# Performance work log

Hardware: AMD Instinct MI355X
Metric: run time of the kernel (lower is better)

The kernel has to match this reference:

```python
import jax, jax.numpy as jnp
import numpy as np

N = 25000          # nodes
E = 400000         # edges (avg degree 16)
H = 64             # hidden_nf
TYPE_DIM = 1
NL = 5             # 4 gcl layers + dgcl_0 (identical shapes, stacked)
GROUP = jnp.array([[[1., 0.], [0., 1.]], [[-1., 0.], [0., -1.]]], dtype=jnp.float32)  # [G,2,2]


def setup_inputs() -> dict:
    key = jax.random.key(0)
    ks = iter(jax.random.split(key, 40))
    def nrm(shape, scale=0.05):
        return jax.random.normal(next(ks), shape, dtype=jnp.float32) * scale
    inp = {}
    inp["nodes"] = nrm((N, 4 + TYPE_DIM), 1.0)
    inp["edges"] = jax.random.randint(next(ks), (2, E), 0, N)
    inp["edge_attr"] = nrm((E, 1), 1.0)
    # embedding: Linear(input_dim, H)
    inp["W_emb"] = nrm((4 + TYPE_DIM, H)); inp["b_emb"] = jnp.zeros((H,), jnp.float32)
    # group_mlp: Linear(G*H, H) -> SiLU -> Linear(H, H)
    G = GROUP.shape[0]
    inp["Wg1"] = nrm((G * H, H)); inp["bg1"] = jnp.zeros((H,), jnp.float32)
    inp["Wg2"] = nrm((H, H));     inp["bg2"] = jnp.zeros((H,), jnp.float32)
    # stacked GCL params for gcl_0..3 + dgcl_0 (all H->H, edges_in_nf=1)
    inp["eW1"] = nrm((NL, 2 * H + 1, H)); inp["eb1"] = jnp.zeros((NL, H), jnp.float32)
    inp["eW2"] = nrm((NL, H, H));         inp["eb2"] = jnp.zeros((NL, H), jnp.float32)
    inp["nW1"] = nrm((NL, 2 * H, H));     inp["nb1"] = jnp.zeros((NL, H), jnp.float32)
    inp["nW2"] = nrm((NL, H, H));         inp["nb2"] = jnp.zeros((NL, H), jnp.float32)
    # dgcl_1: GCL(H, 2*len(group)=4, H)
    inp["deW1"] = nrm((2 * H + 1, H)); inp["deb1"] = jnp.zeros((H,), jnp.float32)
    inp["deW2"] = nrm((H, H));         inp["deb2"] = jnp.zeros((H,), jnp.float32)
    inp["dnW1"] = nrm((2 * H, H));     inp["dnb1"] = jnp.zeros((H,), jnp.float32)
    inp["dnW2"] = nrm((H, 2 * G));     inp["dnb2"] = jnp.zeros((2 * G,), jnp.float32)
    return inp


def _gcl(h, row, col, edge_attr, eW1, eb1, eW2, eb2, nW1, nb1, nW2, nb2):
    # edge model: gather -> MLP (Linear,SiLU,Linear,SiLU)
    e_in = jnp.concatenate([h[row], h[col], edge_attr], axis=1)  # [E, 2H+1]
    e = jax.nn.silu(e_in @ eW1 + eb1)
    e = jax.nn.silu(e @ eW2 + eb2)                               # [E, H]
    # node model: scatter-sum by source index, then MLP (Linear,SiLU,Linear)
    agg = jax.ops.segment_sum(e, row, num_segments=h.shape[0])   # [N, H]
    out = jnp.concatenate([h, agg], axis=1)                      # [N, 2H]
    out = jax.nn.silu(out @ nW1 + nb1) @ nW2 + nb2
    return out  # recurrent=False: no residual


def reference(nodes, edges, edge_attr, W_emb, b_emb, Wg1, bg1, Wg2, bg2,
              eW1, eb1, eW2, eb2, nW1, nb1, nW2, nb2,
              deW1, deb1, deW2, deb2, dnW1, dnb1, dnW2, dnb2):
    loc, vel, ntype = nodes[:, :2], nodes[:, 2:4], nodes[:, 4:]
    # group-equivariant embedding: transform loc/vel by each group element
    loc_g = jnp.einsum('nd,gde->gne', loc, GROUP)   # [G, N, 2]
    vel_g = jnp.einsum('nd,gde->gne', vel, GROUP)   # [G, N, 2]
    ntype_g = jnp.broadcast_to(ntype, (GROUP.shape[0],) + ntype.shape)
    feats = jnp.concatenate([loc_g, vel_g, ntype_g], axis=2)   # [G, N, 5]
    h_g = feats @ W_emb + b_emb                                 # [G, N, H]
    h = jnp.transpose(h_g, (1, 0, 2)).reshape(nodes.shape[0], -1)  # [N, G*H]
    h = jax.nn.silu(h @ Wg1 + bg1) @ Wg2 + bg2
    row, col = edges[0], edges[1]
    for i in range(eW1.shape[0]):  # gcl_0..3 then dgcl_0
        h = _gcl(h, row, col, edge_attr, eW1[i], eb1[i], eW2[i], eb2[i],
                 nW1[i], nb1[i], nW2[i], nb2[i])
    # dgcl_1: node output dim = 2*len(group)
    x = _gcl(h, row, col, edge_attr, deW1, deb1, deW2, deb2,
             dnW1, dnb1, dnW2, dnb2)
    return x
```

## Files before the change

### kernel.cpp

```cpp
#include <hip/hip_runtime.h>
#include <hip/hip_bf16.h>

#define N_NODES 25000
#define N_EDGES 400000
#define NB_SCAN ((N_NODES + 255) / 256)
#define EDGE_TILES (N_EDGES / 16)
#define TPW 3
#define EDGE_WAVES ((EDGE_TILES + TPW - 1) / TPW)
#define EDGE_BLOCKS ((EDGE_WAVES + 3) / 4)
#define NODE_TILES ((N_NODES + 15) / 16)

typedef __attribute__((ext_vector_type(8))) short short8;
typedef __attribute__((ext_vector_type(4))) float f32x4;

__device__ __forceinline__ float silu_f(float x) {
  return x * __builtin_amdgcn_rcpf(1.0f + __expf(-x));
}

__device__ __forceinline__ short f2bf_s(float x) {
  __hip_bfloat16 h = __float2bfloat16(x);
  return *reinterpret_cast<short*>(&h);
}
__device__ __forceinline__ float bf_s2f(short s) {
  __hip_bfloat16 h = *reinterpret_cast<__hip_bfloat16*>(&s);
  return __bfloat162float(h);
}

__device__ __forceinline__ void load_afrag(const float* T, int s, int quad, int n16,
                                           short8& ahi, short8& alo) {
#pragma unroll
  for (int j = 0; j < 8; ++j) {
    float tv = T[(s * 32 + quad * 8 + j) * 17 + n16];
    short hi = f2bf_s(tv);
    ahi[j] = hi;
    alo[j] = f2bf_s(tv - bf_s2f(hi));
  }
}
__device__ __forceinline__ void load_bfrag(const float* __restrict__ W, int k0, int col,
                                           short8& bhi, short8& blo) {
#pragma unroll
  for (int j = 0; j < 8; ++j) {
    float w = W[(k0 + j) * 64 + col];
    short hi = f2bf_s(w);
    bhi[j] = hi;
    blo[j] = f2bf_s(w - bf_s2f(hi));
  }
}
__device__ __forceinline__ f32x4 mfma3(short8 ahi, short8 alo, short8 bhi, short8 blo,
                                       f32x4 acc) {
  acc = __builtin_amdgcn_mfma_f32_16x16x32_bf16(ahi, bhi, acc, 0, 0, 0);
  acc = __builtin_amdgcn_mfma_f32_16x16x32_bf16(ahi, blo, acc, 0, 0, 0);
  acc = __builtin_amdgcn_mfma_f32_16x16x32_bf16(alo, bhi, acc, 0, 0, 0);
  return acc;
}

__global__ __launch_bounds__(256) void k_hist(const int* __restrict__ rows,
                                              int* __restrict__ counts)
{
  int stride = gridDim.x * blockDim.x;
  for (int e = blockIdx.x * blockDim.x + threadIdx.x; e < N_EDGES; e += stride)
    atomicAdd(&counts[rows[e]], 1);
}

__global__ __launch_bounds__(256) void k_scanA(const int* __restrict__ counts,
                                               int* __restrict__ bsum)
{
  __shared__ int sd[256];
  int t = threadIdx.x;
  int i = blockIdx.x * 256 + t;
  int x = (i < N_NODES) ? counts[i] : 0;
  sd[t] = x; __syncthreads();
  for (int d = 128; d > 0; d >>= 1) { if (t < d) sd[t] += sd[t + d]; __syncthreads(); }
  if (t == 0) bsum[blockIdx.x] = sd[0];
}

__global__ __launch_bounds__(128) void k_scanB(const int* __restrict__ bsum,
                                               int* __restrict__ boffs)
{
  __shared__ int buf[128];
  int t = threadIdx.x;
  int x = (t < NB_SCAN) ? bsum[t] : 0;
  buf[t] = x; __syncthreads();
  for (int d = 1; d < 128; d <<= 1) {
    int y = (t >= d) ? buf[t - d] : 0;
    __syncthreads();
    buf[t] += y;
    __syncthreads();
  }
  if (t < NB_SCAN) boffs[t] = buf[t] - x;
}

__global__ __launch_bounds__(256) void k_scanC(const int* __restrict__ counts,
                                               const int* __restrict__ boffs,
                                               int* __restrict__ cursor)
{
  __shared__ int buf[256];
  int t = threadIdx.x;
  int i = blockIdx.x * 256 + t;
  int x = (i < N_NODES) ? counts[i] : 0;
  buf[t] = x; __syncthreads();
  for (int d = 1; d < 256; d <<= 1) {
    int y = (t >= d) ? buf[t - d] : 0;
    __syncthreads();
    buf[t] += y;
    __syncthreads();
  }
  if (i < N_NODES) cursor[i] = boffs[blockIdx.x] + buf[t] - x;
}

__global__ __launch_bounds__(256) void k_scatter(
    const int* __restrict__ rows, const int* __restrict__ cols,
    const float* __restrict__ eatt, int* __restrict__ cursor,
    int* __restrict__ srow, int* __restrict__ scol, float* __restrict__ sea)
{
  int stride = gridDim.x * blockDim.x;
  for (int e = blockIdx.x * blockDim.x + threadIdx.x; e < N_EDGES; e += stride) {
    int r = rows[e];
    int pos = atomicAdd(&cursor[r], 1);
    srow[pos] = r;
    scol[pos] = cols[e];
    sea[pos] = eatt[e];
  }
}

__global__ __launch_bounds__(256, 2) void k_embed_fused(
    const float* __restrict__ nodes,
    const float* __restrict__ W_emb, const float* __restrict__ b_emb,
    const float* __restrict__ Wg1, const float* __restrict__ bg1,
    const float* __restrict__ Wg2, const float* __restrict__ bg2,
    const float* __restrict__ eW1_0, const float* __restrict__ eb1_0,
    float* __restrict__ h, float* __restrict__ u, float* __restrict__ v,
    float* __restrict__ agg)
{
  const int lane = threadIdx.x & 63;
  const int wv = threadIdx.x >> 6;
  const int n16 = lane & 15;
  const int quad = lane >> 4;
  const int col = wv * 16 + n16;

  short8 W1hi[4], W1lo[4], W2hi[2], W2lo[2], Uhi[2], Ulo[2], Vhi[2], Vlo[2];
#pragma unroll
  for (int s = 0; s < 4; ++s)
    load_bfrag(Wg1, s * 32 + quad * 8, col, W1hi[s], W1lo[s]);
#pragma unroll
  for (int s = 0; s < 2; ++s) {
    load_bfrag(Wg2, s * 32 + quad * 8, col, W2hi[s], W2lo[s]);
    load_bfrag(eW1_0, s * 32 + quad * 8, col, Uhi[s], Ulo[s]);
    load_bfrag(eW1_0 + 64 * 64, s * 32 + quad * 8, col, Vhi[s], Vlo[s]);
  }
  float bg1v = bg1[col], bg2v = bg2[col], ebv = eb1_0[col];
  float w0 = W_emb[0 * 64 + lane], w1 = W_emb[1 * 64 + lane],
        w2 = W_emb[2 * 64 + lane], w3 = W_emb[3 * 64 + lane],
        w4 = W_emb[4 * 64 + lane];
  float bev = b_emb[lane];

  __shared__ float Ta[128 * 17];
  __shared__ float Tt[64 * 17];
  __shared__ float Th[64 * 17];
  __shared__ float Tu[64 * 17];
  __shared__ float Tv[64 * 17];

  int n0 = blockIdx.x * 16;
#pragma unroll
  for (int e4 = 0; e4 < 4; ++e4) {
    int e = wv * 4 + e4;
    int n = min(n0 + e, N_NODES - 1);
    float x0 = nodes[n * 5 + 0], x1 = nodes[n * 5 + 1],
          x2 = nodes[n * 5 + 2], x3 = nodes[n * 5 + 3],
          x4 = nodes[n * 5 + 4];
    float base = bev + x4 * w4;
    float sv = x0 * w0 + x1 * w1 + x2 * w2 + x3 * w3;
    Ta[lane * 17 + e] = base + sv;
    Ta[(64 + lane) * 17 + e] = base - sv;
  }
  __syncthreads();

  f32x4 a1 = {};
#pragma unroll
  for (int s = 0; s < 4; ++s) {
    short8 ahi, alo;
    load_afrag(Ta, s, quad, n16, ahi, alo);
    a1 = mfma3(ahi, alo, W1hi[s], W1lo[s], a1);
  }
#pragma unroll
  for (int r = 0; r < 4; ++r)
    Tt[col * 17 + quad * 4 + r] = silu_f(a1[r] + bg1v);
  __syncthreads();

  f32x4 a2 = {};
#pragma unroll
  for (int s = 0; s < 2; ++s) {
    short8 ahi, alo;
    load_afrag(Tt, s, quad, n16, ahi, alo);
    a2 = mfma3(ahi, alo, W2hi[s], W2lo[s], a2);
  }
#pragma unroll
  for (int r = 0; r < 4; ++r)
    Th[col * 17 + quad * 4 + r] = a2[r] + bg2v;
  __syncthreads();

  f32x4 aU = {}, aV = {};
#pragma unroll
  for (int s = 0; s < 2; ++s) {
    short8 ahi, alo;
    load_afrag(Th, s, quad, n16, ahi, alo);
    aU = mfma3(ahi, alo, Uhi[s], Ulo[s], aU);
    aV = mfma3(ahi, alo, Vhi[s], Vlo[s], aV);
  }
#pragma unroll
  for (int r = 0; r < 4; ++r) {
    Tu[col * 17 + quad * 4 + r] = aU[r] + ebv;
    Tv[col * 17 + quad * 4 + r] = aV[r];
  }
  __syncthreads();

#pragma unroll
  for (int e4 = 0; e4 < 4; ++e4) {
    int e = wv * 4 + e4;
    int n = n0 + e;
    if (n < N_NODES) {
      h[n * 64 + lane] = Th[lane * 17 + e];
      u[n * 64 + lane] = Tu[lane * 17 + e];
      v[n * 64 + lane] = Tv[lane * 17 + e];
      agg[n * 64 + lane] = 0.f;
    }
  }
}

__global__ __launch_bounds__(256, 2) void k_postfused(
    float* __restrict__ h, float* __restrict__ agg,
    const float* __restrict__ nW1, const float* __restrict__ nb1,
    const float* __restrict__ nW2, const float* __restrict__ nb2,
    const float* __restrict__ eW1n, const float* __restrict__ eb1n,
    float* __restrict__ u, float* __restrict__ v)
{
  const int lane = threadIdx.x & 63;
  const int wv = threadIdx.x >> 6;
  const int n16 = lane & 15;
  const int quad = lane >> 4;
  const int col = wv * 16 + n16;

  short8 W1hi[4], W1lo[4], W2hi[2], W2lo[2], Uhi[2], Ulo[2], Vhi[2], Vlo[2];
#pragma unroll
  for (int s = 0; s < 4; ++s)
    load_bfrag(nW1, s * 32 + quad * 8, col, W1hi[s], W1lo[s]);
#pragma unroll
  for (int s = 0; s < 2; ++s) {
    load_bfrag(nW2, s * 32 + quad * 8, col, W2hi[s], W2lo[s]);
    load_bfrag(eW1n, s * 32 + quad * 8, col, Uhi[s], Ulo[s]);
    load_bfrag(eW1n + 64 * 64, s * 32 + quad * 8, col, Vhi[s], Vlo[s]);
  }
  float b1 = nb1[col], b2 = nb2[col], ebv = eb1n[col];

  __shared__ float Ta[128 * 17];
  __shared__ float Tt[64 * 17];
  __shared__ float Th[64 * 17];
  __shared__ float Tu[64 * 17];
  __shared__ float Tv[64 * 17];

  int n0 = blockIdx.x * 16;
#pragma unroll
  for (int e4 = 0; e4 < 4; ++e4) {
    int e = wv * 4 + e4;
    int n = min(n0 + e, N_NODES - 1);
    Ta[lane * 17 + e] = h[n * 64 + lane];
    Ta[(64 + lane) * 17 + e] = agg[n * 64 + lane];
  }
  __syncthreads();

  f32x4 a1 = {};
#pragma unroll
  for (int s = 0; s < 4; ++s) {
    short8 ahi, alo;
    load_afrag(Ta, s, quad, n16, ahi, alo);
    a1 = mfma3(ahi, alo, W1hi[s], W1lo[s], a1);
  }
#pragma unroll
  for (int r = 0; r < 4; ++r)
    Tt[col * 17 + quad * 4 + r] = silu_f(a1[r] + b1);
  __syncthreads();

  f32x4 a2 = {};
#pragma unroll
  for (int s = 0; s < 2; ++s) {
    short8 ahi, alo;
    load_afrag(Tt, s, quad, n16, ahi, alo);
    a2 = mfma3(ahi, alo, W2hi[s], W2lo[s], a2);
  }
#pragma unroll
  for (int r = 0; r < 4; ++r)
    Th[col * 17 + quad * 4 + r] = a2[r] + b2;
  __syncthreads();

  f32x4 aU = {}, aV = {};
#pragma unroll
  for (int s = 0; s < 2; ++s) {
    short8 ahi, alo;
    load_afrag(Th, s, quad, n16, ahi, alo);
    aU = mfma3(ahi, alo, Uhi[s], Ulo[s], aU);
    aV = mfma3(ahi, alo, Vhi[s], Vlo[s], aV);
  }
#pragma unroll
  for (int r = 0; r < 4; ++r) {
    Tu[col * 17 + quad * 4 + r] = aU[r] + ebv;
    Tv[col * 17 + quad * 4 + r] = aV[r];
  }
  __syncthreads();

#pragma unroll
  for (int e4 = 0; e4 < 4; ++e4) {
    int e = wv * 4 + e4;
    int n = n0 + e;
    if (n < N_NODES) {
      h[n * 64 + lane] = Th[lane * 17 + e];
      u[n * 64 + lane] = Tu[lane * 17 + e];
      v[n * 64 + lane] = Tv[lane * 17 + e];
      agg[n * 64 + lane] = 0.f;
    }
  }
}

__global__ __launch_bounds__(256) void k_edge(
    const float* __restrict__ u, const float* __restrict__ v,
    const int* __restrict__ srow, const int* __restrict__ scol,
    const float* __restrict__ sea,
    const float* __restrict__ wea,
    const float* __restrict__ W2, const float* __restrict__ eb2,
    float* __restrict__ agg)
{
  const int lane = threadIdx.x & 63;
  const int wv = threadIdx.x >> 6;
  const int n16 = lane & 15;
  const int quad = lane >> 4;

  short8 Whi[2][4], Wlo[2][4];
#pragma unroll
  for (int s = 0; s < 2; ++s) {
#pragma unroll
    for (int nt = 0; nt < 4; ++nt) {
#pragma unroll
      for (int j = 0; j < 8; ++j) {
        float w2v = W2[(s * 32 + quad * 8 + j) * 64 + nt * 16 + n16];
        short hi = f2bf_s(w2v);
        Whi[s][nt][j] = hi;
        Wlo[s][nt][j] = f2bf_s(w2v - bf_s2f(hi));
      }
    }
  }
  float we = wea[lane];
  float b2v[4];
#pragma unroll
  for (int nt = 0; nt < 4; ++nt) b2v[nt] = eb2[nt * 16 + n16];

  __shared__ float Tl[4][64 * 17];
  float* T = Tl[wv];

  const int wid = blockIdx.x * 4 + wv;
  const int tile0 = wid * TPW;
  const int tile1 = min(tile0 + TPW, EDGE_TILES);

  int cur_row = -1;
  bool first_atomic = true;
  float asum[4] = {0.f, 0.f, 0.f, 0.f};

  int r_prev = -1;
  float uval = 0.f;

  auto reduce_pick = [&](float a0, float a1, float a2, float a3) -> float {
    a0 += __shfl_xor(a0, 16); a0 += __shfl_xor(a0, 32);
    a1 += __shfl_xor(a1, 16); a1 += __shfl_xor(a1, 32);
    a2 += __shfl_xor(a2, 16); a2 += __shfl_xor(a2, 32);
    a3 += __shfl_xor(a3, 16); a3 += __shfl_xor(a3, 32);
    float o = a0;
    o = (quad == 1) ? a1 : o;
    o = (quad == 2) ? a2 : o;
    o = (quad == 3) ? a3 : o;
    return o;
  };

  for (int tile = tile0; tile < tile1; ++tile) {
    int e0 = tile * 16;
    int r16a = srow[e0 + n16];
    int c16a = scol[e0 + n16];
    float ea16 = sea[e0 + n16];

    float vv[16];
#pragma unroll
    for (int e = 0; e < 16; ++e) {
      int c = __builtin_amdgcn_readlane(c16a, e);
      vv[e] = v[c * 64 + lane];
    }

#pragma unroll
    for (int e = 0; e < 16; ++e) {
      int r = __builtin_amdgcn_readlane(r16a, e);
      if (r != r_prev) { uval = u[r * 64 + lane]; r_prev = r; }
      float ea = __int_as_float(__builtin_amdgcn_readlane(__float_as_int(ea16), e));
      float tt = uval + vv[e] + ea * we;
      T[lane * 17 + e] = silu_f(tt);
    }
    __builtin_amdgcn_wave_barrier();

    f32x4 acc[4] = {};
#pragma unroll
    for (int s = 0; s < 2; ++s) {
      short8 ahi, alo;
#pragma unroll
      for (int j = 0; j < 8; ++j) {
        float tv = T[(s * 32 + quad * 8 + j) * 17 + n16];
        short hi = f2bf_s(tv);
        ahi[j] = hi;
        alo[j] = f2bf_s(tv - bf_s2f(hi));
      }
#pragma unroll
      for (int nt = 0; nt < 4; ++nt) {
        acc[nt] = __builtin_amdgcn_mfma_f32_16x16x32_bf16(ahi, Whi[s][nt], acc[nt], 0, 0, 0);
        acc[nt] = __builtin_amdgcn_mfma_f32_16x16x32_bf16(ahi, Wlo[s][nt], acc[nt], 0, 0, 0);
        acc[nt] = __builtin_amdgcn_mfma_f32_16x16x32_bf16(alo, Whi[s][nt], acc[nt], 0, 0, 0);
      }
    }
    __builtin_amdgcn_wave_barrier();

    float ev[4][4];
#pragma unroll
    for (int reg = 0; reg < 4; ++reg)
#pragma unroll
      for (int nt = 0; nt < 4; ++nt)
        ev[reg][nt] = silu_f(acc[nt][reg] + b2v[nt]);

    int rup = __shfl_up(r16a, 1);
    bool nf = (lane < 16) && ((lane == 0) ? (r16a != cur_row) : (r16a != rup));
    unsigned mask = (unsigned)(__ballot(nf) & 0xFFFFull);

    int s = 0;
    while (s < 16) {
      if ((mask >> s) & 1u) {
        if (cur_row >= 0) {
          float o = reduce_pick(asum[0], asum[1], asum[2], asum[3]);
          if (first_atomic) { unsafeAtomicAdd(&agg[cur_row * 64 + lane], o); first_atomic = false; }
          else agg[cur_row * 64 + lane] = o;
        }
        asum[0] = asum[1] = asum[2] = asum[3] = 0.f;
        cur_row = __shfl(r16a, s);
      }
      unsigned rem = mask & ~((2u << s) - 1u);
      int e = rem ? (__ffs(rem) - 1) : 16;
#pragma unroll
      for (int reg = 0; reg < 4; ++reg) {
        int m = quad * 4 + reg;
        bool in = (m >= s) && (m < e);
        asum[0] += in ? ev[reg][0] : 0.f;
        asum[1] += in ? ev[reg][1] : 0.f;
        asum[2] += in ? ev[reg][2] : 0.f;
        asum[3] += in ? ev[reg][3] : 0.f;
      }
      s = e;
    }
    __builtin_amdgcn_wave_barrier();
  }

  if (cur_row >= 0) {
    float o = reduce_pick(asum[0], asum[1], asum[2], asum[3]);
    unsafeAtomicAdd(&agg[cur_row * 64 + lane], o);
  }
}

__global__ __launch_bounds__(256, 2) void k_final_mfma(
    const float* __restrict__ h, const float* __restrict__ agg,
    const float* __restrict__ dnW1, const float* __restrict__ dnb1,
    const float* __restrict__ dnW2, const float* __restrict__ dnb2,
    float* __restrict__ out)
{
  const int lane = threadIdx.x & 63;
  const int wv = threadIdx.x >> 6;
  const int n16 = lane & 15;
  const int quad = lane >> 4;
  const int col = wv * 16 + n16;

  short8 W1hi[4], W1lo[4];
#pragma unroll
  for (int s = 0; s < 4; ++s)
    load_bfrag(dnW1, s * 32 + quad * 8, col, W1hi[s], W1lo[s]);
  float b1 = dnb1[col];

  __shared__ float Ta[128 * 17];
  __shared__ float Tt[64 * 17];
  __shared__ float W2s[256];
  __shared__ float Tp[4][64];

  W2s[threadIdx.x] = dnW2[threadIdx.x];

  int n0 = blockIdx.x * 16;
#pragma unroll
  for (int e4 = 0; e4 < 4; ++e4) {
    int e = wv * 4 + e4;
    int n = min(n0 + e, N_NODES - 1);
    Ta[lane * 17 + e] = h[n * 64 + lane];
    Ta[(64 + lane) * 17 + e] = agg[n * 64 + lane];
  }
  __syncthreads();

  f32x4 a1 = {};
#pragma unroll
  for (int s = 0; s < 4; ++s) {
    short8 ahi, alo;
    load_afrag(Ta, s, quad, n16, ahi, alo);
    a1 = mfma3(ahi, alo, W1hi[s], W1lo[s], a1);
  }
#pragma unroll
  for (int r = 0; r < 4; ++r)
    Tt[col * 17 + quad * 4 + r] = silu_f(a1[r] + b1);
  __syncthreads();

  int m = lane >> 2, c = lane & 3;
  float p = 0.f;
#pragma unroll
  for (int kk = 0; kk < 16; ++kk) {
    int k = wv * 16 + kk;
    p += Tt[k * 17 + m] * W2s[k * 4 + c];
  }
  Tp[wv][lane] = p;
  __syncthreads();

  if (threadIdx.x < 64) {
    int n = n0 + (threadIdx.x >> 2);
    if (n < N_NODES) {
      float o = Tp[0][threadIdx.x] + Tp[1][threadIdx.x] +
                Tp[2][threadIdx.x] + Tp[3][threadIdx.x] + dnb2[threadIdx.x & 3];
      out[n * 4 + (threadIdx.x & 3)] = o;
    }
  }
}

extern "C" void kernel_launch(void* const* d_in, const int* in_sizes, int n_in,
                              void* d_out, int out_size, void* d_ws, size_t ws_size,
                              hipStream_t stream)
{
  const float* nodes = (const float*)d_in[0];
  const int*   edges = (const int*)d_in[1];
  const float* eatt  = (const float*)d_in[2];
  const float* W_emb = (const float*)d_in[3];
  const float* b_emb = (const float*)d_in[4];
  const float* Wg1   = (const float*)d_in[5];
  const float* bg1   = (const float*)d_in[6];
  const float* Wg2   = (const float*)d_in[7];
  const float* bg2   = (const float*)d_in[8];
  const float* eW1   = (const float*)d_in[9];
  const float* eb1   = (const float*)d_in[10];
  const float* eW2   = (const float*)d_in[11];
  const float* eb2   = (const float*)d_in[12];
  const float* nW1   = (const float*)d_in[13];
  const float* nb1   = (const float*)d_in[14];
  const float* nW2   = (const float*)d_in[15];
  const float* nb2   = (const float*)d_in[16];
  const float* deW1  = (const float*)d_in[17];
  const float* deb1  = (const float*)d_in[18];
  const float* deW2  = (const float*)d_in[19];
  const float* deb2  = (const float*)d_in[20];
  const float* dnW1  = (const float*)d_in[21];
  const float* dnb1  = (const float*)d_in[22];
  const float* dnW2  = (const float*)d_in[23];
  const float* dnb2  = (const float*)d_in[24];
  float* out = (float*)d_out;

  float* h   = (float*)d_ws;
  float* u   = h + N_NODES * 64;
  float* v   = u + N_NODES * 64;
  float* agg = v + N_NODES * 64;
  int* counts = (int*)(agg + N_NODES * 64);
  int* cursor = counts + N_NODES;
  int* bsum   = cursor + N_NODES;
  int* boffs  = bsum + 128;
  int* srow   = boffs + 128;
  int* scol   = srow + N_EDGES;
  float* sea  = (float*)(scol + N_EDGES);

  const int* rows = edges;
  const int* cols = edges + N_EDGES;

  hipMemsetAsync(counts, 0, N_NODES * sizeof(int), stream);
  k_hist<<<400, 256, 0, stream>>>(rows, counts);
  k_scanA<<<NB_SCAN, 256, 0, stream>>>(counts, bsum);
  k_scanB<<<1, 128, 0, stream>>>(bsum, boffs);
  k_scanC<<<NB_SCAN, 256, 0, stream>>>(counts, boffs, cursor);
  k_scatter<<<400, 256, 0, stream>>>(rows, cols, eatt, cursor, srow, scol, sea);

  k_embed_fused<<<NODE_TILES, 256, 0, stream>>>(nodes, W_emb, b_emb, Wg1, bg1,
                                                Wg2, bg2, eW1, eb1, h, u, v, agg);

  for (int i = 0; i < 5; ++i) {
    const float* W1i = eW1 + i * 129 * 64;
    k_edge<<<EDGE_BLOCKS, 256, 0, stream>>>(u, v, srow, scol, sea, W1i + 128 * 64,
                                            eW2 + i * 64 * 64, eb2 + i * 64, agg);
    const float* eW1next = (i < 4) ? (eW1 + (i + 1) * 129 * 64) : deW1;
    const float* eb1next = (i < 4) ? (eb1 + (i + 1) * 64) : deb1;
    k_postfused<<<NODE_TILES, 256, 0, stream>>>(h, agg,
                                                nW1 + i * 128 * 64, nb1 + i * 64,
                                                nW2 + i * 64 * 64, nb2 + i * 64,
                                                eW1next, eb1next, u, v);
  }
  k_edge<<<EDGE_BLOCKS, 256, 0, stream>>>(u, v, srow, scol, sea, deW1 + 128 * 64,
                                          deW2, deb2, agg);
  k_final_mfma<<<NODE_TILES, 256, 0, stream>>>(h, agg, dnW1, dnb1, dnW2, dnb2, out);
}
```

Measured before the change: 517.8 us.

## Pipeline edge tile gathers, prepack W2 fragments, process two node tiles per block

The edge kernel now handles exactly two tiles per wave and issues the gather of u and v for the second tile before the epilogue of the first, overlapping memory latency with compute. It also drops the per-row u caching. A new prep kernel converts each layer's W2 once into packed bf16 hi/lo MFMA fragments, so edge blocks load short8 vectors instead of converting floats per wave. The node post kernel processes two 16-node tiles per block, reusing the register-held weight fragments and reusing shared buffers. The trade-off is more registers for the double-buffered gathers and redundant u loads, and the code assumes the edge tile count divides evenly by the wave count.

After: 479.1 us. 7.5% less time.

```diff
diff --git a/kernel.cpp b/kernel.cpp
--- a/kernel.cpp
+++ b/kernel.cpp
@@ -5,10 +5,11 @@
 #define N_EDGES 400000
 #define NB_SCAN ((N_NODES + 255) / 256)
 #define EDGE_TILES (N_EDGES / 16)
-#define TPW 3
-#define EDGE_WAVES ((EDGE_TILES + TPW - 1) / TPW)
-#define EDGE_BLOCKS ((EDGE_WAVES + 3) / 4)
+#define TPW 2
+#define EDGE_WAVES (EDGE_TILES / TPW)
+#define EDGE_BLOCKS (EDGE_WAVES / 4)
 #define NODE_TILES ((N_NODES + 15) / 16)
+#define NODE_BLOCKS2 ((NODE_TILES + 1) / 2)
 
 typedef __attribute__((ext_vector_type(8))) short short8;
 typedef __attribute__((ext_vector_type(4))) float f32x4;
@@ -123,6 +124,25 @@
   }
 }
 
+__global__ __launch_bounds__(256) void k_w2prep(const float* __restrict__ eW2,
+                                                const float* __restrict__ deW2,
+                                                short* __restrict__ w2p)
+{
+  int layer = blockIdx.x;
+  const float* src = (layer < 5) ? (eW2 + layer * 64 * 64) : deW2;
+  short* dst = w2p + layer * 8192;
+  for (int t = threadIdx.x; t < 4096; t += 256) {
+    int j = t & 7, n16 = (t >> 3) & 15, quad = (t >> 7) & 3, nt = (t >> 9) & 3,
+        s = (t >> 11) & 1;
+    float val = src[(s * 32 + quad * 8 + j) * 64 + nt * 16 + n16];
+    short hi = f2bf_s(val);
+    short lo = f2bf_s(val - bf_s2f(hi));
+    int base = ((s * 4 + nt) * 4 + quad) * 128 + n16 * 8 + j;
+    dst[base] = hi;
+    dst[base + 4096] = lo;
+  }
+}
+
 __global__ __launch_bounds__(256, 2) void k_embed_fused(
     const float* __restrict__ nodes,
     const float* __restrict__ W_emb, const float* __restrict__ b_emb,
@@ -252,70 +272,87 @@
   }
   float b1 = nb1[col], b2 = nb2[col], ebv = eb1n[col];
 
-  __shared__ float Ta[128 * 17];
-  __shared__ float Tt[64 * 17];
-  __shared__ float Th[64 * 17];
-  __shared__ float Tu[64 * 17];
-  __shared__ float Tv[64 * 17];
-
-  int n0 = blockIdx.x * 16;
-#pragma unroll
-  for (int e4 = 0; e4 < 4; ++e4) {
-    int e = wv * 4 + e4;
-    int n = min(n0 + e, N_NODES - 1);
-    Ta[lane * 17 + e] = h[n * 64 + lane];
-    Ta[(64 + lane) * 17 + e] = agg[n * 64 + lane];
-  }
-  __syncthreads();
-
-  f32x4 a1 = {};
-#pragma unroll
-  for (int s = 0; s < 4; ++s) {
-    short8 ahi, alo;
-    load_afrag(Ta, s, quad, n16, ahi, alo);
-    a1 = mfma3(ahi, alo, W1hi[s], W1lo[s], a1);
-  }
-#pragma unroll
-  for (int r = 0; r < 4; ++r)
-    Tt[col * 17 + quad * 4 + r] = silu_f(a1[r] + b1);
-  __syncthreads();
-
-  f32x4 a2 = {};
-#pragma unroll
-  for (int s = 0; s < 2; ++s) {
-    short8 ahi, alo;
-    load_afrag(Tt, s, quad, n16, ahi, alo);
-    a2 = mfma3(ahi, alo, W2hi[s], W2lo[s], a2);
-  }
-#pragma unroll
-  for (int r = 0; r < 4; ++r)
-    Th[col * 17 + quad * 4 + r] = a2[r] + b2;
-  __syncthreads();
-
-  f32x4 aU = {}, aV = {};
-#pragma unroll
-  for (int s = 0; s < 2; ++s) {
-    short8 ahi, alo;
-    load_afrag(Th, s, quad, n16, ahi, alo);
-    aU = mfma3(ahi, alo, Uhi[s], Ulo[s], aU);
-    aV = mfma3(ahi, alo, Vhi[s], Vlo[s], aV);
-  }
-#pragma unroll
-  for (int r = 0; r < 4; ++r) {
-    Tu[col * 17 + quad * 4 + r] = aU[r] + ebv;
-    Tv[col * 17 + quad * 4 + r] = aV[r];
-  }
-  __syncthreads();
-
-#pragma unroll
-  for (int e4 = 0; e4 < 4; ++e4) {
-    int e = wv * 4 + e4;
-    int n = n0 + e;
-    if (n < N_NODES) {
-      h[n * 64 + lane] = Th[lane * 17 + e];
-      u[n * 64 + lane] = Tu[lane * 17 + e];
-      v[n * 64 + lane] = Tv[lane * 17 + e];
-      agg[n * 64 + lane] = 0.f;
+  __shared__ float LA[2][128 * 17];
+  __shared__ float LB[2][64 * 17];
+
+  int t0 = blockIdx.x * 2;
+#pragma unroll
+  for (int q = 0; q < 2; ++q) {
+    int n0 = (t0 + q) * 16;
+#pragma unroll
+    for (int e4 = 0; e4 < 4; ++e4) {
+      int e = wv * 4 + e4;
+      int n = min(n0 + e, N_NODES - 1);
+      LA[q][lane * 17 + e] = h[n * 64 + lane];
+      LA[q][(64 + lane) * 17 + e] = agg[n * 64 + lane];
+    }
+  }
+  __syncthreads();
+
+  f32x4 a1[2] = {};
+#pragma unroll
+  for (int q = 0; q < 2; ++q)
+#pragma unroll
+    for (int s = 0; s < 4; ++s) {
+      short8 ahi, alo;
+      load_afrag(LA[q], s, quad, n16, ahi, alo);
+      a1[q] = mfma3(ahi, alo, W1hi[s], W1lo[s], a1[q]);
+    }
+#pragma unroll
+  for (int q = 0; q < 2; ++q)
+#pragma unroll
+    for (int r = 0; r < 4; ++r)
+      LB[q][col * 17 + quad * 4 + r] = silu_f(a1[q][r] + b1);
+  __syncthreads();
+
+  f32x4 a2[2] = {};
+#pragma unroll
+  for (int q = 0; q < 2; ++q)
+#pragma unroll
+    for (int s = 0; s < 2; ++s) {
+      short8 ahi, alo;
+      load_afrag(LB[q], s, quad, n16, ahi, alo);
+      a2[q] = mfma3(ahi, alo, W2hi[s], W2lo[s], a2[q]);
+    }
+#pragma unroll
+  for (int q = 0; q < 2; ++q)
+#pragma unroll
+    for (int r = 0; r < 4; ++r)
+      LA[q][col * 17 + quad * 4 + r] = a2[q][r] + b2;
+  __syncthreads();
+
+  f32x4 aU[2] = {}, aV[2] = {};
+#pragma unroll
+  for (int q = 0; q < 2; ++q)
+#pragma unroll
+    for (int s = 0; s < 2; ++s) {
+      short8 ahi, alo;
+      load_afrag(LA[q], s, quad, n16, ahi, alo);
+      aU[q] = mfma3(ahi, alo, Uhi[s], Ulo[s], aU[q]);
+      aV[q] = mfma3(ahi, alo, Vhi[s], Vlo[s], aV[q]);
+    }
+#pragma unroll
+  for (int q = 0; q < 2; ++q)
+#pragma unroll
+    for (int r = 0; r < 4; ++r) {
+      LA[q][1088 + col * 17 + quad * 4 + r] = aU[q][r] + ebv;
+      LB[q][col * 17 + quad * 4 + r] = aV[q][r];
+    }
+  __syncthreads();
+
+#pragma unroll
+  for (int q = 0; q < 2; ++q) {
+    int n0 = (t0 + q) * 16;
+#pragma unroll
+    for (int e4 = 0; e4 < 4; ++e4) {
+      int e = wv * 4 + e4;
+      int n = n0 + e;
+      if (n < N_NODES) {
+        h[n * 64 + lane] = LA[q][lane * 17 + e];
+        u[n * 64 + lane] = LA[q][1088 + lane * 17 + e];
+        v[n * 64 + lane] = LB[q][lane * 17 + e];
+        agg[n * 64 + lane] = 0.f;
+      }
     }
   }
 }
@@ -325,7 +362,7 @@
     const int* __restrict__ srow, const int* __restrict__ scol,
     const float* __restrict__ sea,
     const float* __restrict__ wea,
-    const float* __restrict__ W2, const float* __restrict__ eb2,
+    const short* __restrict__ w2p, const float* __restrict__ eb2,
     float* __restrict__ agg)
 {
   const int lane = threadIdx.x & 63;
@@ -333,20 +370,15 @@
   const int n16 = lane & 15;
   const int quad = lane >> 4;
 
+  const short8* Wp8 = reinterpret_cast<const short8*>(w2p);
   short8 Whi[2][4], Wlo[2][4];
 #pragma unroll
-  for (int s = 0; s < 2; ++s) {
+  for (int s = 0; s < 2; ++s)
 #pragma unroll
     for (int nt = 0; nt < 4; ++nt) {
-#pragma unroll
-      for (int j = 0; j < 8; ++j) {
-        float w2v = W2[(s * 32 + quad * 8 + j) * 64 + nt * 16 + n16];
-        short hi = f2bf_s(w2v);
-        Whi[s][nt][j] = hi;
-        Wlo[s][nt][j] = f2bf_s(w2v - bf_s2f(hi));
-      }
-    }
-  }
+      Whi[s][nt] = Wp8[((s * 4 + nt) * 4 + quad) * 16 + n16];
+      Wlo[s][nt] = Wp8[((s * 4 + nt) * 4 + quad) * 16 + n16 + 512];
+    }
   float we = wea[lane];
   float b2v[4];
 #pragma unroll
@@ -357,14 +389,10 @@
 
   const int wid = blockIdx.x * 4 + wv;
   const int tile0 = wid * TPW;
-  const int tile1 = min(tile0 + TPW, EDGE_TILES);
 
   int cur_row = -1;
   bool first_atomic = true;
   float asum[4] = {0.f, 0.f, 0.f, 0.f};
-
-  int r_prev = -1;
-  float uval = 0.f;
 
   auto reduce_pick = [&](float a0, float a1, float a2, float a3) -> float {
     a0 += __shfl_xor(a0, 16); a0 += __shfl_xor(a0, 32);
@@ -378,30 +406,24 @@
     return o;
   };
 
-  for (int tile = tile0; tile < tile1; ++tile) {
-    int e0 = tile * 16;
-    int r16a = srow[e0 + n16];
-    int c16a = scol[e0 + n16];
-    float ea16 = sea[e0 + n16];
-
-    float vv[16];
-#pragma unroll
-    for (int e = 0; e < 16; ++e) {
-      int c = __builtin_amdgcn_readlane(c16a, e);
-      vv[e] = v[c * 64 + lane];
-    }
-
+  auto gather = [&](int r16a, int c16a, float (&uuT)[16], float (&vvT)[16]) {
 #pragma unroll
     for (int e = 0; e < 16; ++e) {
       int r = __builtin_amdgcn_readlane(r16a, e);
-      if (r != r_prev) { uval = u[r * 64 + lane]; r_prev = r; }
-      float ea = __int_as_float(__builtin_amdgcn_readlane(__float_as_int(ea16), e));
-      float tt = uval + vv[e] + ea * we;
-      T[lane * 17 + e] = silu_f(tt);
+      int c = __builtin_amdgcn_readlane(c16a, e);
+      uuT[e] = u[r * 64 + lane];
+      vvT[e] = v[c * 64 + lane];
+    }
+  };
+
+  auto phase1_mfma = [&](float ea16v, const float (&uuT)[16], const float (&vvT)[16],
+                         f32x4 (&acc)[4]) {
+#pragma unroll
+    for (int e = 0; e < 16; ++e) {
+      float ea = __int_as_float(__builtin_amdgcn_readlane(__float_as_int(ea16v), e));
+      T[lane * 17 + e] = silu_f(uuT[e] + vvT[e] + ea * we);
     }
     __builtin_amdgcn_wave_barrier();
-
-    f32x4 acc[4] = {};
 #pragma unroll
     for (int s = 0; s < 2; ++s) {
       short8 ahi, alo;
@@ -420,7 +442,9 @@
       }
     }
     __builtin_amdgcn_wave_barrier();
-
+  };
+
+  auto epilogue = [&](int r16a, f32x4 (&acc)[4]) {
     float ev[4][4];
 #pragma unroll
     for (int reg = 0; reg < 4; ++reg)
@@ -457,7 +481,29 @@
       s = e;
     }
     __builtin_amdgcn_wave_barrier();
-  }
+  };
+
+  int e0 = tile0 * 16;
+  int rA = srow[e0 + n16], cA = scol[e0 + n16];
+  float eA = sea[e0 + n16];
+  float uuA[16], vvA[16];
+  gather(rA, cA, uuA, vvA);
+
+  int e1 = e0 + 16;
+  int rB = srow[e1 + n16], cB = scol[e1 + n16];
+  float eB = sea[e1 + n16];
+
+  f32x4 accA[4] = {};
+  phase1_mfma(eA, uuA, vvA, accA);
+
+  float uuB[16], vvB[16];
+  gather(rB, cB, uuB, vvB);
+
+  epilogue(rA, accA);
+
+  f32x4 accB[4] = {};
+  phase1_mfma(eB, uuB, vvB, accB);
+  epilogue(rB, accB);
 
   if (cur_row >= 0) {
     float o = reduce_pick(asum[0], asum[1], asum[2], asum[3]);
@@ -574,11 +620,13 @@
   int* srow   = boffs + 128;
   int* scol   = srow + N_EDGES;
   float* sea  = (float*)(scol + N_EDGES);
+  short* w2p  = (short*)(sea + N_EDGES);
 
   const int* rows = edges;
   const int* cols = edges + N_EDGES;
 
   hipMemsetAsync(counts, 0, N_NODES * sizeof(int), stream);
+  k_w2prep<<<6, 256, 0, stream>>>(eW2, deW2, w2p);
   k_hist<<<400, 256, 0, stream>>>(rows, counts);
   k_scanA<<<NB_SCAN, 256, 0, stream>>>(counts, bsum);
   k_scanB<<<1, 128, 0, stream>>>(bsum, boffs);
@@ -589,17 +637,17 @@
                                                 Wg2, bg2, eW1, eb1, h, u, v, agg);
 
   for (int i = 0; i < 5; ++i) {
-    const float* W1i = eW1 + i * 129 * 64;
-    k_edge<<<EDGE_BLOCKS, 256, 0, stream>>>(u, v, srow, scol, sea, W1i + 128 * 64,
-                                            eW2 + i * 64 * 64, eb2 + i * 64, agg);
+    k_edge<<<EDGE_BLOCKS, 256, 0, stream>>>(u, v, srow, scol, sea,
+                                            eW1 + i * 129 * 64 + 128 * 64,
+                                            w2p + i * 8192, eb2 + i * 64, agg);
     const float* eW1next = (i < 4) ? (eW1 + (i + 1) * 129 * 64) : deW1;
     const float* eb1next = (i < 4) ? (eb1 + (i + 1) * 64) : deb1;
-    k_postfused<<<NODE_TILES, 256, 0, stream>>>(h, agg,
-                                                nW1 + i * 128 * 64, nb1 + i * 64,
-                                                nW2 + i * 64 * 64, nb2 + i * 64,
-                                                eW1next, eb1next, u, v);
+    k_postfused<<<NODE_BLOCKS2, 256, 0, stream>>>(h, agg,
+                                                  nW1 + i * 128 * 64, nb1 + i * 64,
+                                                  nW2 + i * 64 * 64, nb2 + i * 64,
+                                                  eW1next, eb1next, u, v);
   }
   k_edge<<<EDGE_BLOCKS, 256, 0, stream>>>(u, v, srow, scol, sea, deW1 + 128 * 64,
-                                          deW2, deb2, agg);
+                                          w2p + 5 * 8192, deb2, agg);
   k_final_mfma<<<NODE_TILES, 256, 0, stream>>>(h, agg, dnW1, dnb1, dnW2, dnb2, out);
 }
```
